# Optimization experiments

Hardware: AMD Instinct MI355X
Metric: run time of the kernel (lower is better)

## Reference

```python
import jax, jax.numpy as jnp
import numpy as np
import math

B, S, HID = 1, 2048, 2048
H, QLR, KVLR = 16, 1536, 512
NOPE, ROPE, VD = 128, 64, 128
QKD = NOPE + ROPE


def rmsnorm(x, w, eps=1e-6):
    v = jnp.mean(x * x, axis=-1, keepdims=True)
    return w * (x * jax.lax.rsqrt(v + eps))


def rope_tables(seq_len, dim):
    inv_freq = 1.0 / (10000.0 ** (jnp.arange(0, dim, 2, dtype=jnp.float32) / dim))
    t = jnp.arange(seq_len, dtype=jnp.float32)[:, None]
    freqs = t * inv_freq[None, :]
    freqs = jnp.concatenate([freqs, freqs], axis=-1)  # [S, dim]
    return jnp.cos(freqs), jnp.sin(freqs)


def rotate_half(x):
    x1, x2 = jnp.split(x, 2, axis=-1)
    return jnp.concatenate([-x2, x1], axis=-1)


def setup_inputs() -> dict:
    key = jax.random.key(0)
    ks = jax.random.split(key, 8)
    s = 0.02
    return {
        'x': jax.random.normal(ks[0], (B, S, HID), jnp.float32),
        'wq_a_w': jax.random.normal(ks[1], (QLR, HID), jnp.float32) * s,
        'wq_a_b': jnp.zeros((QLR,), jnp.float32),
        'q_norm_w': jnp.ones((QLR,), jnp.float32),
        'wq_b_w': jax.random.normal(ks[2], (H * QKD, QLR), jnp.float32) * s,
        'wq_b_b': jnp.zeros((H * QKD,), jnp.float32),
        'wkv_a_w': jax.random.normal(ks[3], (KVLR + ROPE, HID), jnp.float32) * s,
        'wkv_a_b': jnp.zeros((KVLR + ROPE,), jnp.float32),
        'kv_norm_w': jnp.ones((KVLR,), jnp.float32),
        'wkv_b_w': jax.random.normal(ks[4], (H * (NOPE + VD), KVLR), jnp.float32) * s,
        'wo_w': jax.random.normal(ks[5], (HID, H * VD), jnp.float32) * s,
        'wo_b': jnp.zeros((HID,), jnp.float32),
    }


def reference(x, wq_a_w, wq_a_b, q_norm_w, wq_b_w, wq_b_b, wkv_a_w, wkv_a_b,
              kv_norm_w, wkv_b_w, wo_w, wo_b):
    bs, seq_len, _ = x.shape
    # low-rank q projection
    q = x @ wq_a_w.T + wq_a_b            # [B,S,QLR]
    q = rmsnorm(q, q_norm_w)
    q = q @ wq_b_w.T + wq_b_b            # [B,S,H*QKD]
    q = q.reshape(bs, seq_len, H, QKD)
    q_nope, q_pe = q[..., :NOPE], q[..., NOPE:]

    # latent kv + rope key
    kv_full = x @ wkv_a_w.T + wkv_a_b    # [B,S,KVLR+ROPE]
    kv, k_pe = kv_full[..., :KVLR], kv_full[..., KVLR:]

    cos, sin = rope_tables(seq_len, ROPE)        # [S,ROPE]
    cos4 = cos[None, :, None, :]
    sin4 = sin[None, :, None, :]
    q_pe = q_pe * cos4 + rotate_half(q_pe) * sin4          # [B,S,H,ROPE]
    k_pe = k_pe * cos[None] + rotate_half(k_pe) * sin[None]  # [B,S,ROPE]

    # absorbed kv projection
    wkv_b = wkv_b_w.reshape(H, NOPE + VD, KVLR)
    q_nope = jnp.einsum('bshd,hdc->bshc', q_nope, wkv_b[:, :NOPE])  # [B,S,H,KVLR]
    kv = rmsnorm(kv, kv_norm_w)                                     # [B,T,KVLR]

    scores = (jnp.einsum('bshc,btc->bsht', q_nope, kv)
              + jnp.einsum('bshr,btr->bsht', q_pe, k_pe)) / math.sqrt(QKD)
    # causal mask: position t > s masked
    s_idx = jnp.arange(seq_len)
    mask = jnp.where(s_idx[None, :, None, None] >= s_idx[None, None, None, :],
                     0.0, -jnp.inf)  # [1,S,1,T]
    scores = jax.nn.softmax(scores + mask, axis=-1)

    out = jnp.einsum('bsht,btc->bshc', scores, kv)            # [B,S,H,KVLR]
    out = jnp.einsum('bshc,hdc->bshd', out, wkv_b[:, NOPE:])  # [B,S,H,VD]
    out = out.reshape(bs, seq_len, H * VD)
    return out @ wo_w.T + wo_b
```

## Files before the change

### kernel.cpp

```cpp
#include <hip/hip_runtime.h>
#include <hip/hip_bf16.h>
#include <stdint.h>


using bf16 = __hip_bfloat16;
typedef __bf16 bf16x8 __attribute__((ext_vector_type(8)));
typedef __bf16 bf16x4 __attribute__((ext_vector_type(4)));
typedef float f32x4 __attribute__((ext_vector_type(4)));

#define S_LEN 2048
#define NHEAD 16

static __device__ __forceinline__ void gload16(const void* g, void* l) {
  __builtin_amdgcn_global_load_lds(
      (const __attribute__((address_space(1))) unsigned int*)g,
      (__attribute__((address_space(3))) unsigned int*)l, 16, 0, 0);
}

__global__ void cvt_all(const float* __restrict__ x, const float* __restrict__ wqa_s,
                        const float* __restrict__ wqb_s, const float* __restrict__ wkva_s,
                        const float* __restrict__ wkvb_s, const float* __restrict__ wo_s,
                        bf16* __restrict__ xb, bf16* __restrict__ wqa,
                        bf16* __restrict__ wqb, bf16* __restrict__ wkva,
                        bf16* __restrict__ wkvb, bf16* __restrict__ wob) {
  const size_t n0 = 1048576;
  const size_t n1 = n0 + 786432;
  const size_t n2 = n1 + 1179648;
  const size_t n3 = n2 + 327680;
  const size_t n4 = n3 + 524288;
  const size_t n5 = n4 + 1048576;
  auto cvt4 = [](const float4 v, bf16* d) {
    bf16x4 o;
    o[0] = (__bf16)__float2bfloat16(v.x);
    o[1] = (__bf16)__float2bfloat16(v.y);
    o[2] = (__bf16)__float2bfloat16(v.z);
    o[3] = (__bf16)__float2bfloat16(v.w);
    *(bf16x4*)d = o;
  };
  for (size_t i = (size_t)blockIdx.x * blockDim.x + threadIdx.x; i < n5;
       i += (size_t)gridDim.x * blockDim.x) {
    if (i < n0) {
      cvt4(*(const float4*)(x + i * 4), xb + i * 4);
    } else if (i < n1) {
      size_t j = i - n0;
      cvt4(*(const float4*)(wqa_s + j * 4), wqa + j * 4);
    } else if (i < n2) {
      size_t j = i - n1;
      cvt4(*(const float4*)(wqb_s + j * 4), wqb + j * 4);
    } else if (i < n3) {
      size_t j = i - n2;
      size_t e = j * 4;
      int r = (int)(e / 2048), c = (int)(e % 2048);
      float4 v = (r < 576) ? *(const float4*)(wkva_s + (size_t)r * 2048 + c)
                           : make_float4(0.f, 0.f, 0.f, 0.f);
      cvt4(v, wkva + e);
    } else if (i < n4) {
      size_t j = i - n3;
      cvt4(*(const float4*)(wkvb_s + j * 4), wkvb + j * 4);
    } else {
      size_t j = i - n4;
      cvt4(*(const float4*)(wo_s + j * 4), wob + j * 4);
    }
  }
}

__global__ void rmsnorm_bf16(const bf16* __restrict__ in, const float* __restrict__ w,
                             bf16* __restrict__ out, int cols) {
  const int r = blockIdx.x, tid = threadIdx.x;
  const bf16* row = in + (size_t)r * cols;
  float ss = 0.f;
  for (int c = tid; c < cols; c += 256) {
    float v = __bfloat162float(row[c]);
    ss += v * v;
  }
  for (int m = 32; m >= 1; m >>= 1) ss += __shfl_xor(ss, m, 64);
  __shared__ float red[4];
  if ((tid & 63) == 0) red[tid >> 6] = ss;
  __syncthreads();
  ss = red[0] + red[1] + red[2] + red[3];
  float inv = rsqrtf(ss / (float)cols + 1e-6f);
  for (int c = tid; c < cols; c += 256)
    out[(size_t)r * cols + c] = __float2bfloat16(__bfloat162float(row[c]) * inv * w[c]);
}

__global__ void kv_post(const float* __restrict__ kvf, const float* __restrict__ kvw,
                        bf16* __restrict__ kvn, bf16* __restrict__ Kh) {
  const int t = blockIdx.x, tid = threadIdx.x;
  const float* row = kvf + (size_t)t * 640;
  float ss = 0.f;
  for (int c = tid; c < 512; c += 256) { float v = row[c]; ss += v * v; }
  for (int m = 32; m >= 1; m >>= 1) ss += __shfl_xor(ss, m, 64);
  __shared__ float red[4];
  if ((tid & 63) == 0) red[tid >> 6] = ss;
  __syncthreads();
  ss = red[0] + red[1] + red[2] + red[3];
  float inv = rsqrtf(ss * (1.0f / 512.0f) + 1e-6f);
  for (int c = tid; c < 512; c += 256)
    kvn[(size_t)t * 512 + c] = __float2bfloat16(row[c] * inv * kvw[c]);
  if (tid < 32) {
    const int j = tid;
    float freq = expf(-(float)j * (1.0f / 32.0f) * 9.210340371976184f);
    float ang = (float)t * freq;
    float cs = cosf(ang), sn = sinf(ang);
    float x1 = row[512 + j];
    float x2 = row[512 + j + 32];
    bf16 o1 = __float2bfloat16(x1 * cs - x2 * sn);
    bf16 o2 = __float2bfloat16(x2 * cs + x1 * sn);
#pragma unroll
    for (int h = 0; h < 16; ++h) {
      bf16* kr = Kh + ((size_t)h * S_LEN + t) * 192 + 128;
      kr[j] = o1;
      kr[j + 32] = o2;
    }
  }
}

__global__ void q_rope(bf16* __restrict__ qv) {
  const int s = blockIdx.x, tid = threadIdx.x;
  for (int it = tid; it < 512; it += 256) {
    const int h = it >> 5, j = it & 31;
    float freq = expf(-(float)j * (1.0f / 32.0f) * 9.210340371976184f);
    float ang = (float)s * freq;
    float cs = cosf(ang), sn = sinf(ang);
    bf16* base = qv + (size_t)s * 3072 + h * 192 + 128;
    float x1 = __bfloat162float(base[j]);
    float x2 = __bfloat162float(base[j + 32]);
    base[j] = __float2bfloat16(x1 * cs - x2 * sn);
    base[j + 32] = __float2bfloat16(x2 * cs + x1 * sn);
  }
}

__global__ void softmax_rows(bf16* __restrict__ S) {
  const int q = blockIdx.x, hh = blockIdx.y;
  bf16* row = S + ((size_t)hh * S_LEN + q) * S_LEN;
  const int tid = threadIdx.x, w = tid >> 6, lane = tid & 63;
  const int i0 = tid * 8;
  const int padend = ((q >> 7) + 1) << 7;
  __shared__ float red[4];
  bf16x8 in = {};
  if (i0 < padend) in = *(const bf16x8*)(row + i0);
  const float scale = 0.0721687836487032f;
  float v[8];
  float mx = -3e38f;
#pragma unroll
  for (int j = 0; j < 8; ++j) {
    v[j] = (i0 + j <= q) ? (float)in[j] * scale : -3e38f;
    mx = fmaxf(mx, v[j]);
  }
#pragma unroll
  for (int d = 1; d < 64; d <<= 1) mx = fmaxf(mx, __shfl_xor(mx, d, 64));
  if (lane == 0) red[w] = mx;
  __syncthreads();
  mx = fmaxf(fmaxf(red[0], red[1]), fmaxf(red[2], red[3]));
  __syncthreads();
  float p[8], sum = 0.f;
#pragma unroll
  for (int j = 0; j < 8; ++j) {
    p[j] = (i0 + j <= q) ? __expf(v[j] - mx) : 0.f;
    sum += p[j];
  }
#pragma unroll
  for (int d = 1; d < 64; d <<= 1) sum += __shfl_xor(sum, d, 64);
  if (lane == 0) red[w] = sum;
  __syncthreads();
  sum = red[0] + red[1] + red[2] + red[3];
  const float inv = 1.0f / sum;
  if (i0 < padend) {
    bf16x8 o8;
#pragma unroll
    for (int j = 0; j < 8; ++j) o8[j] = (__bf16)__float2bfloat16(p[j] * inv);
    *(bf16x8*)(row + i0) = o8;
  }
}

template <bool BIAS, bool BF16OUT, int BM>
__global__ __launch_bounds__(256)
void gemm_bt(const bf16* __restrict__ A, const bf16* __restrict__ B,
             const float* __restrict__ bias, void* __restrict__ Cv,
             int lda, int ldb, int ldc, int K, int Nreal,
             long long bA, long long bB, long long bC, int mode) {
  int bx, byi, bz;
  {
    const int gx = gridDim.x, gy = gridDim.y;
    const int nwg = gx * gy * (int)gridDim.z;
    const int lin = (int)blockIdx.x + gx * ((int)blockIdx.y + gy * (int)blockIdx.z);
    const int cpx = nwg >> 3;
    const int l2 = (lin & 7) * cpx + (lin >> 3);
    bx = l2 % gx;
    byi = (l2 / gx) % gy;
    bz = l2 / (gx * gy);
    if (mode) byi = (bz & 1) ? byi : gy - 1 - byi;
  }
  const size_t m0 = (size_t)byi * BM, n0 = (size_t)bx * 128;
  if (mode == 1 && (int)n0 >= (int)m0 + BM) return;
  const int Keff = (mode == 2) ? ((K < (int)m0 + BM) ? K : (int)m0 + BM) : K;

  constexpr int ACH = BM / 8;
  constexpr int PER = (ACH + 16) / 4;
  constexpr int NFR = (BM == 64) ? 2 : 4;
  __shared__ bf16 As[2][BM * 64];
  __shared__ bf16 Bs[2][8192];
  const int tid = threadIdx.x;
  const int wave = tid >> 6, lane = tid & 63;
  const int lo = lane & 15, hi = lane >> 4;
  const int rowbase = (BM == 64) ? 0 : ((wave >> 1) * 64);
  const int colbase = (BM == 64) ? (wave * 32) : ((wave & 1) * 64);
  A += (size_t)bz * (size_t)bA;
  B += (size_t)bz * (size_t)bB;
  const int srow = lane >> 3;
  const int scol = (((lane & 7) ^ srow) * 8);
  const int rsw = lo & 7;

  auto stage = [&](int k0, int buf) {
#pragma unroll
    for (int i = 0; i < PER; ++i) {
      const int blk = wave * PER + i;
      if (blk < ACH) {
        const int row = blk * 8 + srow;
        gload16(A + (m0 + row) * (size_t)lda + k0 + scol, &As[buf][blk * 512]);
      } else {
        const int j = blk - ACH;
        const int row = j * 8 + srow;
        gload16(B + (n0 + row) * (size_t)ldb + k0 + scol, &Bs[buf][j * 512]);
      }
    }
  };

  f32x4 acc[4][NFR] = {};
  stage(0, 0);
  int cur = 0;
  for (int k0 = 0; k0 < Keff; k0 += 64) {
    __syncthreads();
    if (k0 + 64 < Keff) stage(k0 + 64, cur ^ 1);
#pragma unroll
    for (int kk = 0; kk < 2; ++kk) {
      const int ch = (((kk << 2) + hi) ^ rsw) << 3;
      bf16x8 af[4], bfr[NFR];
#pragma unroll
      for (int m = 0; m < 4; ++m)
        af[m] = *(const bf16x8*)&As[cur][(rowbase + m * 16 + lo) * 64 + ch];
#pragma unroll
      for (int n = 0; n < NFR; ++n)
        bfr[n] = *(const bf16x8*)&Bs[cur][(colbase + n * 16 + lo) * 64 + ch];
#pragma unroll
      for (int m = 0; m < 4; ++m)
#pragma unroll
        for (int n = 0; n < NFR; ++n)
          acc[m][n] = __builtin_amdgcn_mfma_f32_16x16x32_bf16(af[m], bfr[n], acc[m][n], 0, 0, 0);
    }
    cur ^= 1;
  }
  float* Cf = (float*)Cv;
  bf16* Cb = (bf16*)Cv;
  const size_t cbase = (size_t)bz * (size_t)bC;
#pragma unroll
  for (int m = 0; m < 4; ++m) {
    const size_t row = m0 + rowbase + m * 16 + hi * 4;
#pragma unroll
    for (int n = 0; n < NFR; ++n) {
      const int col = (int)n0 + colbase + n * 16 + lo;
      if (col < Nreal) {
        const float bv = BIAS ? bias[col] : 0.0f;
#pragma unroll
        for (int j = 0; j < 4; ++j) {
          const float v = acc[m][n][j] + bv;
          const size_t off = cbase + (row + j) * (size_t)ldc + col;
          if (BF16OUT) Cb[off] = __float2bfloat16(v);
          else         Cf[off] = v;
        }
      }
    }
  }
}

extern "C" void kernel_launch(void* const* d_in, const int* in_sizes, int n_in,
                              void* d_out, int out_size, void* d_ws, size_t ws_size,
                              hipStream_t stream) {
  const float* x       = (const float*)d_in[0];
  const float* wq_a_w  = (const float*)d_in[1];
  const float* wq_a_b  = (const float*)d_in[2];
  const float* q_norm  = (const float*)d_in[3];
  const float* wq_b_w  = (const float*)d_in[4];
  const float* wq_b_b  = (const float*)d_in[5];
  const float* wkv_a_w = (const float*)d_in[6];
  const float* wkv_a_b = (const float*)d_in[7];
  const float* kv_norm = (const float*)d_in[8];
  const float* wkv_b_w = (const float*)d_in[9];
  const float* wo_w    = (const float*)d_in[10];
  const float* wo_bias = (const float*)d_in[11];
  float* out = (float*)d_out;

  char* base = (char*)d_ws;
  bf16*  Sbuf = (bf16*)(base);
  bf16*  xb   = (bf16*)(base + 0);
  bf16*  wqa  = (bf16*)(base + 8388608);
  bf16*  wqb  = (bf16*)(base + 14680064);
  bf16*  wkva = (bf16*)(base + 24117248);
  bf16*  wkvb = (bf16*)(base + 26738688);
  bf16*  qa   = (bf16*)(base + 30932992);
  bf16*  qn   = (bf16*)(base + 37224448);
  float* kvf  = (float*)(base + 43515904);
  bf16*  kvn  = (bf16*)(base + 48758784);
  char* q = base + 134217728;
  bf16* qv   = (bf16*)(q);             q += 12582912;
  bf16* Kh   = (bf16*)(q);             q += 12582912;
  bf16* V2T  = (bf16*)(q);             q += 8388608;
  bf16* wob  = (bf16*)(q);             q += 8388608;
  bf16* oabs = (bf16*)(q);             q += 8388608;

  cvt_all<<<dim3(2048), 256, 0, stream>>>(x, wq_a_w, wq_b_w, wkv_a_w, wkv_b_w, wo_w,
                                          xb, wqa, wqb, wkva, wkvb, wob);

  gemm_bt<true, true, 64><<<dim3(12, 32, 1), 256, 0, stream>>>(
      xb, wqa, wq_a_b, qa, 2048, 2048, 1536, 2048, 1536, 0, 0, 0, 0);
  rmsnorm_bf16<<<2048, 256, 0, stream>>>(qa, q_norm, qn, 1536);
  gemm_bt<true, true, 128><<<dim3(24, 16, 1), 256, 0, stream>>>(
      qn, wqb, wq_b_b, qv, 1536, 1536, 3072, 1536, 3072, 0, 0, 0, 0);
  q_rope<<<2048, 256, 0, stream>>>(qv);
  gemm_bt<true, false, 64><<<dim3(5, 32, 1), 256, 0, stream>>>(
      xb, wkva, wkv_a_b, kvf, 2048, 2048, 640, 2048, 576, 0, 0, 0, 0);
  kv_post<<<2048, 256, 0, stream>>>(kvf, kv_norm, kvn, Kh);
  gemm_bt<false, true, 64><<<dim3(1, 32, 16), 256, 0, stream>>>(
      kvn, wkvb, nullptr, Kh, 512, 512, 192, 512, 128,
      0, 256ll * 512, 2048ll * 192, 0);
  gemm_bt<false, true, 64><<<dim3(16, 2, 16), 256, 0, stream>>>(
      wkvb + 128ull * 512, kvn, nullptr, V2T, 512, 512, 2048, 512, 2048,
      256ll * 512, 0, 128ll * 2048, 0);

  gemm_bt<false, true, 128><<<dim3(16, 16, 16), 256, 0, stream>>>(
      qv, Kh, nullptr, Sbuf,
      3072, 192, 2048, 192, 2048,
      192ll, 2048ll * 192, 2048ll * 2048, 1);
  softmax_rows<<<dim3(2048, 16), 256, 0, stream>>>(Sbuf);
  gemm_bt<false, true, 64><<<dim3(1, 32, 16), 256, 0, stream>>>(
      Sbuf, V2T, nullptr, oabs,
      2048, 2048, 2048, 2048, 128,
      2048ll * 2048, 128ll * 2048, 128ll, 2);

  gemm_bt<true, false, 64><<<dim3(16, 32, 1), 256, 0, stream>>>(
      oabs, wob, wo_bias, out, 2048, 2048, 2048, 2048, 2048, 0, 0, 0, 0);
}
```

Measured before the change: 252.4 us.

## Fuse QK^T, causal softmax and PV into a single flash-attention kernel

Replaces the three-stage attention (score GEMM writing a full S×S bf16 matrix per head, row softmax, then P·V GEMM) with one flash-attention kernel. It uses online softmax, double-buffered K/V tiles loaded into LDS via global_load_lds, and MFMA for both products, with reverse query-block ordering to balance causal work. This removes the large score-matrix round trip through memory and two launches. The trade-off is small 32-key tiles and per-wave rescaling overhead, which may leave MFMA utilization low.

```diff
diff --git a/kernel.cpp b/kernel.cpp
--- a/kernel.cpp
+++ b/kernel.cpp
@@ -130,47 +130,153 @@
   }
 }
 
-__global__ void softmax_rows(bf16* __restrict__ S) {
-  const int q = blockIdx.x, hh = blockIdx.y;
-  bf16* row = S + ((size_t)hh * S_LEN + q) * S_LEN;
+__global__ __launch_bounds__(256, 3)
+void attn_flash(const bf16* __restrict__ qv, const bf16* __restrict__ Kh,
+                const bf16* __restrict__ V2T, bf16* __restrict__ oabs) {
+  const int lin = (int)blockIdx.x + 32 * (int)blockIdx.y;
+  const int l2 = (lin & 7) * 64 + (lin >> 3);
+  const int h = l2 >> 5;
+  const int qb = 31 - (l2 & 31);
   const int tid = threadIdx.x, w = tid >> 6, lane = tid & 63;
-  const int i0 = tid * 8;
-  const int padend = ((q >> 7) + 1) << 7;
-  __shared__ float red[4];
-  bf16x8 in = {};
-  if (i0 < padend) in = *(const bf16x8*)(row + i0);
-  const float scale = 0.0721687836487032f;
-  float v[8];
-  float mx = -3e38f;
-#pragma unroll
-  for (int j = 0; j < 8; ++j) {
-    v[j] = (i0 + j <= q) ? (float)in[j] * scale : -3e38f;
-    mx = fmaxf(mx, v[j]);
-  }
-#pragma unroll
-  for (int d = 1; d < 64; d <<= 1) mx = fmaxf(mx, __shfl_xor(mx, d, 64));
-  if (lane == 0) red[w] = mx;
-  __syncthreads();
-  mx = fmaxf(fmaxf(red[0], red[1]), fmaxf(red[2], red[3]));
-  __syncthreads();
-  float p[8], sum = 0.f;
-#pragma unroll
-  for (int j = 0; j < 8; ++j) {
-    p[j] = (i0 + j <= q) ? __expf(v[j] - mx) : 0.f;
-    sum += p[j];
-  }
-#pragma unroll
-  for (int d = 1; d < 64; d <<= 1) sum += __shfl_xor(sum, d, 64);
-  if (lane == 0) red[w] = sum;
-  __syncthreads();
-  sum = red[0] + red[1] + red[2] + red[3];
-  const float inv = 1.0f / sum;
-  if (i0 < padend) {
-    bf16x8 o8;
-#pragma unroll
-    for (int j = 0; j < 8; ++j) o8[j] = (__bf16)__float2bfloat16(p[j] * inv);
-    *(bf16x8*)(row + i0) = o8;
-  }
+  const int lo = lane & 15, hi = lane >> 4;
+  __shared__ bf16 Kn[2][32 * 128];
+  __shared__ bf16 Kr[2][32 * 64];
+  __shared__ bf16 Vt[2][128 * 32];
+  __shared__ bf16 Pl[4][16 * 40];
+  const int q0 = qb * 64 + w * 16;
+  const int q = q0 + lo;
+
+  bf16x8 Qf[6];
+  {
+    const bf16* qp = qv + (size_t)(q0 + lo) * 3072 + h * 192 + hi * 8;
+#pragma unroll
+    for (int ks = 0; ks < 6; ++ks) Qf[ks] = *(const bf16x8*)(qp + ks * 32);
+  }
+  f32x4 o[8];
+#pragma unroll
+  for (int cg = 0; cg < 8; ++cg) o[cg] = (f32x4){0.f, 0.f, 0.f, 0.f};
+  float mrow = -3e38f, lrow = 0.f;
+
+  const bf16* khh = Kh + (size_t)h * S_LEN * 192;
+  const bf16* vth = V2T + (size_t)h * 128 * S_LEN;
+
+  auto stage = [&](int tt, int b) {
+    const int t0s = tt * 32;
+#pragma unroll
+    for (int i = 0; i < 2; ++i) {
+      const int c = w * 2 + i;
+      const int row = c * 4 + (lane >> 4);
+      gload16(khh + (size_t)(t0s + row) * 192 + (((lane & 15) ^ (row & 7)) << 3),
+              &Kn[b][c * 512]);
+    }
+#pragma unroll
+    for (int i = 0; i < 2; ++i) {
+      const int c = w * 2 + i;
+      const int row = c * 16 + (lane >> 2);
+      gload16(vth + (size_t)row * S_LEN + t0s + ((lane & 3) << 3),
+              &Vt[b][c * 512]);
+    }
+    {
+      const int row = w * 8 + (lane >> 3);
+      gload16(khh + (size_t)(t0s + row) * 192 + 128 + ((((lane & 7) ^ (row & 7))) << 3),
+              &Kr[b][w * 512]);
+    }
+  };
+
+  const int ntile = 2 * qb + 2;
+  stage(0, 0);
+  for (int t = 0; t < ntile; ++t) {
+    __syncthreads();
+    const int b = t & 1;
+    if (t + 1 < ntile) stage(t + 1, b ^ 1);
+    const int t0 = t * 32;
+
+    f32x4 sc[2];
+    sc[0] = (f32x4){0.f, 0.f, 0.f, 0.f};
+    sc[1] = (f32x4){0.f, 0.f, 0.f, 0.f};
+#pragma unroll
+    for (int ks = 0; ks < 4; ++ks)
+#pragma unroll
+      for (int f = 0; f < 2; ++f) {
+        const int row = f * 16 + lo;
+        bf16x8 kf = *(const bf16x8*)&Kn[b][row * 128 + (((ks << 2) + hi) ^ (lo & 7)) * 8];
+        sc[f] = __builtin_amdgcn_mfma_f32_16x16x32_bf16(kf, Qf[ks], sc[f], 0, 0, 0);
+      }
+#pragma unroll
+    for (int kk2 = 0; kk2 < 2; ++kk2)
+#pragma unroll
+      for (int f = 0; f < 2; ++f) {
+        const int row = f * 16 + lo;
+        bf16x8 kf = *(const bf16x8*)&Kr[b][row * 64 + (((kk2 << 2) + hi) ^ (lo & 7)) * 8];
+        sc[f] = __builtin_amdgcn_mfma_f32_16x16x32_bf16(kf, Qf[4 + kk2], sc[f], 0, 0, 0);
+      }
+
+    const bool diag = (t0 + 31 > q0);
+    float rmax = -3e38f;
+#pragma unroll
+    for (int f = 0; f < 2; ++f)
+#pragma unroll
+      for (int j = 0; j < 4; ++j) {
+        float v = sc[f][j] * 0.0721687836487032f;
+        if (diag && (t0 + f * 16 + hi * 4 + j > q)) v = -3e38f;
+        sc[f][j] = v;
+        rmax = fmaxf(rmax, v);
+      }
+    rmax = fmaxf(rmax, __shfl_xor(rmax, 16, 64));
+    rmax = fmaxf(rmax, __shfl_xor(rmax, 32, 64));
+
+    const float mn = fmaxf(mrow, rmax);
+    const float fsc = __expf(mrow - mn);
+    mrow = mn;
+
+    float rsum = 0.f;
+    bf16* prow = &Pl[w][lo * 40];
+#pragma unroll
+    for (int f = 0; f < 2; ++f) {
+      float pj[4];
+#pragma unroll
+      for (int j = 0; j < 4; ++j) {
+        pj[j] = __expf(sc[f][j] - mn);
+        rsum += pj[j];
+      }
+#pragma unroll
+      for (int i2 = 0; i2 < 2; ++i2) {
+        uint32_t lo16 = (uint32_t)__bfloat16_as_ushort(__float2bfloat16(pj[i2 * 2]));
+        uint32_t hi16 = (uint32_t)__bfloat16_as_ushort(__float2bfloat16(pj[i2 * 2 + 1]));
+        *(uint32_t*)(prow + f * 16 + hi * 4 + i2 * 2) = lo16 | (hi16 << 16);
+      }
+    }
+    rsum += __shfl_xor(rsum, 16, 64);
+    rsum += __shfl_xor(rsum, 32, 64);
+    lrow = lrow * fsc + rsum;
+
+    float fscO[4];
+#pragma unroll
+    for (int j = 0; j < 4; ++j) fscO[j] = __shfl(fsc, hi * 4 + j, 64);
+#pragma unroll
+    for (int cg = 0; cg < 8; ++cg)
+#pragma unroll
+      for (int j = 0; j < 4; ++j) o[cg][j] *= fscO[j];
+
+    bf16x8 pa = *(const bf16x8*)&Pl[w][lo * 40 + hi * 8];
+#pragma unroll
+    for (int cg = 0; cg < 8; ++cg) {
+      bf16x8 vf = *(const bf16x8*)&Vt[b][(cg * 16 + lo) * 32 + hi * 8];
+      o[cg] = __builtin_amdgcn_mfma_f32_16x16x32_bf16(pa, vf, o[cg], 0, 0, 0);
+    }
+  }
+
+  const float linv = 1.0f / lrow;
+  float linvO[4];
+#pragma unroll
+  for (int j = 0; j < 4; ++j) linvO[j] = __shfl(linv, hi * 4 + j, 64);
+  bf16* ob = oabs + (size_t)q0 * 2048 + h * 128;
+#pragma unroll
+  for (int j = 0; j < 4; ++j)
+#pragma unroll
+    for (int cg = 0; cg < 8; ++cg)
+      ob[(size_t)(hi * 4 + j) * 2048 + cg * 16 + lo] =
+          __float2bfloat16(o[cg][j] * linvO[j]);
 }
 
 template <bool BIAS, bool BF16OUT, int BM>
@@ -291,7 +397,6 @@
   float* out = (float*)d_out;
 
   char* base = (char*)d_ws;
-  bf16*  Sbuf = (bf16*)(base);
   bf16*  xb   = (bf16*)(base + 0);
   bf16*  wqa  = (bf16*)(base + 8388608);
   bf16*  wqb  = (bf16*)(base + 14680064);
@@ -327,15 +432,7 @@
       wkvb + 128ull * 512, kvn, nullptr, V2T, 512, 512, 2048, 512, 2048,
       256ll * 512, 0, 128ll * 2048, 0);
 
-  gemm_bt<false, true, 128><<<dim3(16, 16, 16), 256, 0, stream>>>(
-      qv, Kh, nullptr, Sbuf,
-      3072, 192, 2048, 192, 2048,
-      192ll, 2048ll * 192, 2048ll * 2048, 1);
-  softmax_rows<<<dim3(2048, 16), 256, 0, stream>>>(Sbuf);
-  gemm_bt<false, true, 64><<<dim3(1, 32, 16), 256, 0, stream>>>(
-      Sbuf, V2T, nullptr, oabs,
-      2048, 2048, 2048, 2048, 128,
-      2048ll * 2048, 128ll * 2048, 128ll, 2);
+  attn_flash<<<dim3(32, 16), 256, 0, stream>>>(qv, Kh, V2T, oabs);
 
   gemm_bt<true, false, 64><<<dim3(16, 32, 1), 256, 0, stream>>>(
       oabs, wob, wo_bias, out, 2048, 2048, 2048, 2048, 2048, 0, 0, 0, 0);
```

New measurement: 258.7 us. +2.5%, slower.
